# Kernel tuning notes

Measured on AMD Instinct MI355X. Metric: run time of the kernel, lower is better.

Reference implementation:

```python
import jax, jax.numpy as jnp
import numpy as np

MUL_S, MUL_V = 256, 128              # 256x0e + 128x1o hidden irreps
DIM_H = MUL_S + 3 * MUL_V            # 640
N_NODES = 100000
INV_SQRT3 = 3.0 ** -0.5
# e3nn 'element' path normalization: sqrt(ir_out.dim / sum_paths(mul1*mul2));
# for the 1o output the extra sqrt(3) cancels the 1/sqrt(3) of the wigner-3j,
# so every path ends up with the same constant.
C0 = (1.0 / (MUL_S + MUL_V)) ** 0.5


def _unif(key, shape, fan):
    # matches linear_layer_init: uniform(-a, a), a = sqrt(6/(mul1*mul2 + mul_out)), mul2 = 1
    a = (6.0 / fan) ** 0.5
    return jax.random.uniform(key, shape, minval=-a, maxval=a, dtype=jnp.float32)


def setup_inputs() -> dict:
    key = jax.random.key(0)
    ks = jax.random.split(key, 8)
    data_in = jax.random.normal(ks[0], (N_NODES, DIM_H + 4), dtype=jnp.float32)
    return {
        "data_in": data_in,
        "W_ss": _unif(ks[1], (MUL_S, MUL_S), MUL_S + MUL_S),      # 0e x 0e -> 0e (scalars)
        "W_vv": _unif(ks[2], (MUL_V, MUL_S), MUL_V + MUL_S),      # 1o x 1o -> 0e (scalars)
        "W_ss_g": _unif(ks[3], (MUL_S, MUL_V), MUL_S + MUL_V),    # 0e x 0e -> 0e (gates)
        "W_vv_g": _unif(ks[4], (MUL_V, MUL_V), MUL_V + MUL_V),    # 1o x 1o -> 0e (gates)
        "W_sv": _unif(ks[5], (MUL_S, MUL_V), MUL_S + MUL_V),      # 0e x 1o -> 1o
        "W_vs": _unif(ks[6], (MUL_V, MUL_V), MUL_V + MUL_V),      # 1o x 0e -> 1o
        "b": jnp.zeros((MUL_S,), dtype=jnp.float32),
    }


def reference(data_in, W_ss, W_vv, W_ss_g, W_vv_g, W_sv, W_vs, b):
    # split hidden / pos parts (forward does data_in[:, :-irreps_pos.dim] etc.)
    xs = data_in[:, :MUL_S]                           # [N, 256] 0e
    xv = data_in[:, MUL_S:DIM_H].reshape(-1, MUL_V, 3)  # [N, 128, 3] 1o
    ps = data_in[:, DIM_H:DIM_H + 1]                  # [N, 1] pos scalar
    pv = data_in[:, DIM_H + 1:]                       # [N, 3] pos vector

    # CG invariants feeding the 0e outputs
    s0 = xs * ps                                       # 0e x 0e path
    dot = jnp.einsum('nuk,nk->nu', xv, pv) * INV_SQRT3  # 1o x 1o -> 0e path, [N, 128]

    scal = C0 * (s0 @ W_ss + dot @ W_vv) + b           # [N, 256] scalars (+bias on N_trivial)
    gate = C0 * (s0 @ W_ss_g + dot @ W_vv_g)           # [N, 128] gates

    # 1o outputs: 0e x 1o and 1o x 0e paths
    v1 = (xs @ W_sv)[:, :, None] * pv[:, None, :]            # [N, 128, 3]
    v2 = jnp.einsum('nuk,uw->nwk', xv, W_vs) * ps[:, :, None]  # [N, 128, 3]
    vec = C0 * (v1 + v2)

    # Gate: Swish(beta=1) on scalars, sigmoid(gates) multiplying gated 1o irreps
    scal_out = scal * jax.nn.sigmoid(scal)
    vec_out = vec * jax.nn.sigmoid(gate)[:, :, None]
    return jnp.concatenate([scal_out, vec_out.reshape(-1, 3 * MUL_V)], axis=1)  # [N, 640]
```

## Files before the change

kernel.cpp:

```cpp
#include <hip/hip_runtime.h>
#include <hip/hip_bf16.h>

#define MUL_Sc 256
#define DIM_Hc 640
#define IN_COLS 644
#define KF 768
#define NT 64

#define C0F 0.05103103630798287f
#define INV_SQRT3F 0.57735026918962576f

typedef __attribute__((ext_vector_type(8))) short short8;
typedef __attribute__((ext_vector_type(4))) float f32x4;

#define MFMA(a, b, c) __builtin_amdgcn_mfma_f32_16x16x32_bf16((a), (b), (c), 0, 0, 0)

__device__ __forceinline__ unsigned short f2bf(float x) {
    union { float f; unsigned u; } v; v.f = x;
    unsigned r = v.u + 0x7fffu + ((v.u >> 16) & 1u);
    return (unsigned short)(r >> 16);
}

__global__ void prep_weights(const float* __restrict__ Wss, const float* __restrict__ Wvv,
                             const float* __restrict__ Wssg, const float* __restrict__ Wvvg,
                             const float* __restrict__ Wsv, const float* __restrict__ Wvs,
                             unsigned short* __restrict__ wt) {
    int i = blockIdx.x * 256 + threadIdx.x;
    const int N_SG = 384 * 384;
    const int N_SV = 128 * 256;
    const int N_VS = 128 * 128;
    if (i < N_SG) {
        int col = i / 384, k = i % 384;
        float v;
        if (col < 256) v = (k < 256) ? Wss[k * 256 + col] : Wvv[(k - 256) * 256 + col];
        else { int c = col - 256; v = (k < 256) ? Wssg[k * 128 + c] : Wvvg[(k - 256) * 128 + c]; }
        wt[i] = f2bf(v);
    } else if (i < N_SG + N_SV) {
        int j = i - N_SG; int col = j >> 8, k = j & 255;
        wt[i] = f2bf(Wsv[k * 128 + col]);
    } else if (i < N_SG + N_SV + N_VS) {
        int j = i - N_SG - N_SV; int col = j >> 7, k = j & 127;
        wt[i] = f2bf(Wvs[k * 128 + col]);
    }
}

__global__ __launch_bounds__(512, 2)
void fused_main(const float* __restrict__ din, const unsigned short* __restrict__ wt,
                const float* __restrict__ bias, float* __restrict__ out, int N) {
    __shared__ unsigned short feat[NT * KF];
    __shared__ float psv[NT * 4];

    const int tid = threadIdx.x;
    const int n0 = blockIdx.x * NT;

    {
        const int g = tid >> 3;
        const int j = tid & 7;
        int n = n0 + g; if (n >= N) n = N - 1;
        const float* row = din + (size_t)n * IN_COLS;
        float ps  = row[DIM_Hc];
        float pv0 = row[DIM_Hc + 1], pv1 = row[DIM_Hc + 2], pv2 = row[DIM_Hc + 3];
        if (j == 0) { psv[g*4+0] = ps; psv[g*4+1] = pv0; psv[g*4+2] = pv1; psv[g*4+3] = pv2; }
        char* fb = (char*)feat;
        const int swz  = (g & 7) << 4;
        const int rowb = g * (KF * 2);

        #pragma unroll
        for (int half = 0; half < 2; ++half) {
            int c = 32 * j + 16 * half;
            float4 x0 = *(const float4*)(row + c);
            float4 x1 = *(const float4*)(row + c + 4);
            float4 x2 = *(const float4*)(row + c + 8);
            float4 x3 = *(const float4*)(row + c + 12);
            short8 p0, p1;
            p0[0]=(short)f2bf(x0.x); p0[1]=(short)f2bf(x0.y); p0[2]=(short)f2bf(x0.z); p0[3]=(short)f2bf(x0.w);
            p0[4]=(short)f2bf(x1.x); p0[5]=(short)f2bf(x1.y); p0[6]=(short)f2bf(x1.z); p0[7]=(short)f2bf(x1.w);
            p1[0]=(short)f2bf(x2.x); p1[1]=(short)f2bf(x2.y); p1[2]=(short)f2bf(x2.z); p1[3]=(short)f2bf(x2.w);
            p1[4]=(short)f2bf(x3.x); p1[5]=(short)f2bf(x3.y); p1[6]=(short)f2bf(x3.z); p1[7]=(short)f2bf(x3.w);
            *(short8*)(fb + ((rowb + c * 2) ^ swz))       = p0;
            *(short8*)(fb + ((rowb + (c + 8) * 2) ^ swz)) = p1;
        }
        #pragma unroll
        for (int half = 0; half < 2; ++half) {
            int u0 = 16 * j + 8 * half;
            const float* p = row + MUL_Sc + 3 * u0;
            float e[24];
            #pragma unroll
            for (int q = 0; q < 6; ++q) {
                float4 v = *(const float4*)(p + 4 * q);
                e[4*q+0] = v.x; e[4*q+1] = v.y; e[4*q+2] = v.z; e[4*q+3] = v.w;
            }
            short8 dp, k0, k1, k2;
            #pragma unroll
            for (int m = 0; m < 8; ++m) {
                float a = e[3*m], b = e[3*m+1], c = e[3*m+2];
                dp[m] = (short)f2bf((a * pv0 + b * pv1 + c * pv2) * INV_SQRT3F);
                k0[m] = (short)f2bf(a);
                k1[m] = (short)f2bf(b);
                k2[m] = (short)f2bf(c);
            }
            *(short8*)(fb + ((rowb + (256 + u0) * 2) ^ swz)) = dp;
            *(short8*)(fb + ((rowb + (384 + u0) * 2) ^ swz)) = k0;
            *(short8*)(fb + ((rowb + (512 + u0) * 2) ^ swz)) = k1;
            *(short8*)(fb + ((rowb + (640 + u0) * 2) ^ swz)) = k2;
        }
    }
    __syncthreads();

    const int wave = tid >> 6;
    const int lane = tid & 63;
    const int l15  = lane & 15;
    const int lkb  = (lane >> 4) << 3;
    const int rbase = (lane >> 4) << 2;
    const char* fbr = (const char*)feat;
    const int swzr = (l15 & 7) << 4;

    const unsigned short* WTsg = wt;
    const unsigned short* WTsv = wt + 384 * 384;
    const unsigned short* WTvs = wt + 384 * 384 + 128 * 256;

    float pss[4][4];
    #pragma unroll
    for (int m = 0; m < 4; ++m)
    #pragma unroll
    for (int i = 0; i < 4; ++i) pss[m][i] = psv[(m * 16 + rbase + i) * 4];

    f32x4 accS[3][4];
    #pragma unroll
    for (int t = 0; t < 3; ++t)
    #pragma unroll
    for (int m = 0; m < 4; ++m) accS[t][m] = (f32x4){0,0,0,0};

    #pragma unroll
    for (int ks = 0; ks < 8; ++ks) {
        int kf = ks * 32 + lkb;
        short8 a[4];
        #pragma unroll
        for (int m = 0; m < 4; ++m)
            a[m] = *(const short8*)(fbr + (((m * 16 + l15) * 1536 + kf * 2) ^ swzr));
        #pragma unroll
        for (int t = 0; t < 3; ++t) {
            int ct = wave + t * 8;
            short8 b = *(const short8*)(WTsg + (ct * 16 + l15) * 384 + ks * 32 + lkb);
            #pragma unroll
            for (int m = 0; m < 4; ++m) accS[t][m] = MFMA(a[m], b, accS[t][m]);
        }
    }
    #pragma unroll
    for (int t = 0; t < 3; ++t)
    #pragma unroll
    for (int m = 0; m < 4; ++m)
    #pragma unroll
    for (int i = 0; i < 4; ++i) accS[t][m][i] *= pss[m][i];
    #pragma unroll
    for (int ks = 0; ks < 4; ++ks) {
        int kf = 256 + ks * 32 + lkb;
        short8 a[4];
        #pragma unroll
        for (int m = 0; m < 4; ++m)
            a[m] = *(const short8*)(fbr + (((m * 16 + l15) * 1536 + kf * 2) ^ swzr));
        #pragma unroll
        for (int t = 0; t < 3; ++t) {
            int ct = wave + t * 8;
            short8 b = *(const short8*)(WTsg + (ct * 16 + l15) * 384 + 256 + ks * 32 + lkb);
            #pragma unroll
            for (int m = 0; m < 4; ++m) accS[t][m] = MFMA(a[m], b, accS[t][m]);
        }
    }

    #pragma unroll
    for (int t = 0; t < 2; ++t) {
        int col = (wave + t * 8) * 16 + l15;
        float bc = bias[col];
        #pragma unroll
        for (int m = 0; m < 4; ++m)
        #pragma unroll
        for (int i = 0; i < 4; ++i) {
            int n = n0 + m * 16 + rbase + i;
            if (n < N) {
                float sc = C0F * accS[t][m][i] + bc;
                out[(size_t)n * DIM_Hc + col] = sc / (1.f + __expf(-sc));
            }
        }
    }
    float sgr[4][4];
    #pragma unroll
    for (int m = 0; m < 4; ++m)
    #pragma unroll
    for (int i = 0; i < 4; ++i) sgr[m][i] = 1.f / (1.f + __expf(-C0F * accS[2][m][i]));

    f32x4 accA[4], accV[3][4];
    #pragma unroll
    for (int m = 0; m < 4; ++m) accA[m] = (f32x4){0,0,0,0};
    #pragma unroll
    for (int k = 0; k < 3; ++k)
    #pragma unroll
    for (int m = 0; m < 4; ++m) accV[k][m] = (f32x4){0,0,0,0};

    #pragma unroll
    for (int ks = 0; ks < 8; ++ks) {
        int kf = ks * 32 + lkb;
        short8 b = *(const short8*)(WTsv + (wave * 16 + l15) * 256 + ks * 32 + lkb);
        #pragma unroll
        for (int m = 0; m < 4; ++m) {
            short8 a = *(const short8*)(fbr + (((m * 16 + l15) * 1536 + kf * 2) ^ swzr));
            accA[m] = MFMA(a, b, accA[m]);
        }
    }
    #pragma unroll
    for (int ks = 0; ks < 4; ++ks) {
        short8 b = *(const short8*)(WTvs + (wave * 16 + l15) * 128 + ks * 32 + lkb);
        #pragma unroll
        for (int p = 0; p < 3; ++p) {
            int kf = 384 + 128 * p + ks * 32 + lkb;
            #pragma unroll
            for (int m = 0; m < 4; ++m) {
                short8 a = *(const short8*)(fbr + (((m * 16 + l15) * 1536 + kf * 2) ^ swzr));
                accV[p][m] = MFMA(a, b, accV[p][m]);
            }
        }
    }

    {
        int u = wave * 16 + l15;
        #pragma unroll
        for (int m = 0; m < 4; ++m)
        #pragma unroll
        for (int i = 0; i < 4; ++i) {
            int nl = m * 16 + rbase + i;
            int n = n0 + nl;
            if (n >= N) continue;
            float sg  = sgr[m][i];
            float ps  = pss[m][i];
            float pv0 = psv[nl * 4 + 1], pv1 = psv[nl * 4 + 2], pv2 = psv[nl * 4 + 3];
            float av = accA[m][i];
            size_t ob = (size_t)n * DIM_Hc + MUL_Sc + 3 * u;
            out[ob + 0] = C0F * (av * pv0 + accV[0][m][i] * ps) * sg;
            out[ob + 1] = C0F * (av * pv1 + accV[1][m][i] * ps) * sg;
            out[ob + 2] = C0F * (av * pv2 + accV[2][m][i] * ps) * sg;
        }
    }
}

extern "C" void kernel_launch(void* const* d_in, const int* in_sizes, int n_in,
                              void* d_out, int out_size, void* d_ws, size_t ws_size,
                              hipStream_t stream) {
    const float* din  = (const float*)d_in[0];
    const float* Wss  = (const float*)d_in[1];
    const float* Wvv  = (const float*)d_in[2];
    const float* Wssg = (const float*)d_in[3];
    const float* Wvvg = (const float*)d_in[4];
    const float* Wsv  = (const float*)d_in[5];
    const float* Wvs  = (const float*)d_in[6];
    const float* bias = (const float*)d_in[7];
    float* out = (float*)d_out;
    unsigned short* wt = (unsigned short*)d_ws;

    const size_t WT_BYTES = (size_t)(384 * 384 + 128 * 256 + 128 * 128) * 2;
    if (ws_size < WT_BYTES) return;

    int N = in_sizes[0] / IN_COLS;

    int prep_total = 384 * 384 + 128 * 256 + 128 * 128;
    prep_weights<<<(prep_total + 255) / 256, 256, 0, stream>>>(Wss, Wvv, Wssg, Wvvg, Wsv, Wvs, wt);

    int nblocks = (N + NT - 1) / NT;
    fused_main<<<nblocks, 512, 0, stream>>>(din, wt, bias, out, N);
}
```

Measured before the change: 234.5 us.

## Make fused kernel persistent with double-buffered LDS and register prefetch of next tile

Switches from one 64-node block per tile to a persistent grid of 256 blocks that walk 32-node tiles. While the current tile runs its MFMA work, the next tile's input row is prefetched into registers, then converted to bf16 into the other LDS buffer. The aim is to hide global load latency behind compute and cut per-block setup overhead. The cost is smaller M tiles (half the MFMA reuse of each B fragment loaded from global), higher register pressure from the prefetch registers, and a grid of only 256 blocks, which may leave compute units underused with 2 blocks per CU allowed.

Measured after the change: 449.5 us. 91.7% more time.

```diff
diff --git a/kernel.cpp b/kernel.cpp
--- a/kernel.cpp
+++ b/kernel.cpp
@@ -5,7 +5,8 @@
 #define DIM_Hc 640
 #define IN_COLS 644
 #define KF 768
-#define NT 64
+#define NT 32
+#define GRIDB 256
 
 #define C0F 0.05103103630798287f
 #define INV_SQRT3F 0.57735026918962576f
@@ -46,32 +47,54 @@
 
 __global__ __launch_bounds__(512, 2)
 void fused_main(const float* __restrict__ din, const unsigned short* __restrict__ wt,
-                const float* __restrict__ bias, float* __restrict__ out, int N) {
-    __shared__ unsigned short feat[NT * KF];
-    __shared__ float psv[NT * 4];
+                const float* __restrict__ bias, float* __restrict__ out,
+                int N, int ntiles) {
+    __shared__ unsigned short feat[2][NT * KF];
+    __shared__ float psv[2][NT * 4];
 
     const int tid = threadIdx.x;
-    const int n0 = blockIdx.x * NT;
-
-    {
-        const int g = tid >> 3;
-        const int j = tid & 7;
-        int n = n0 + g; if (n >= N) n = N - 1;
+    const int g = tid >> 4;
+    const int j = tid & 15;
+
+    const int wave = tid >> 6;
+    const int lane = tid & 63;
+    const int l15  = lane & 15;
+    const int lkb  = (lane >> 4) << 3;
+    const int rbase = (lane >> 4) << 2;
+    const int swzr = (l15 & 7) << 4;
+
+    const unsigned short* WTsg = wt;
+    const unsigned short* WTsv = wt + 384 * 384;
+    const unsigned short* WTvs = wt + 384 * 384 + 128 * 256;
+
+    float bc0 = bias[(wave)     * 16 + l15];
+    float bc1 = bias[(wave + 8) * 16 + l15];
+
+    float4 xs4[4], xv4[6], pp;
+
+    auto issue = [&](int tile) {
+        int n = tile * NT + g; if (n >= N) n = N - 1;
         const float* row = din + (size_t)n * IN_COLS;
-        float ps  = row[DIM_Hc];
-        float pv0 = row[DIM_Hc + 1], pv1 = row[DIM_Hc + 2], pv2 = row[DIM_Hc + 3];
-        if (j == 0) { psv[g*4+0] = ps; psv[g*4+1] = pv0; psv[g*4+2] = pv1; psv[g*4+3] = pv2; }
-        char* fb = (char*)feat;
+        #pragma unroll
+        for (int q = 0; q < 4; ++q) xs4[q] = *(const float4*)(row + 16 * j + 4 * q);
+        #pragma unroll
+        for (int q = 0; q < 6; ++q) xv4[q] = *(const float4*)(row + MUL_Sc + 24 * j + 4 * q);
+        pp = *(const float4*)(row + DIM_Hc);
+    };
+
+    auto convertw = [&](int wb) {
+        char* fb = (char*)&feat[wb][0];
         const int swz  = (g & 7) << 4;
         const int rowb = g * (KF * 2);
-
-        #pragma unroll
-        for (int half = 0; half < 2; ++half) {
-            int c = 32 * j + 16 * half;
-            float4 x0 = *(const float4*)(row + c);
-            float4 x1 = *(const float4*)(row + c + 4);
-            float4 x2 = *(const float4*)(row + c + 8);
-            float4 x3 = *(const float4*)(row + c + 12);
+        float ps = pp.x, pv0 = pp.y, pv1 = pp.z, pv2 = pp.w;
+        (void)ps;
+        if (j == 0) {
+            psv[wb][g*4+0] = pp.x; psv[wb][g*4+1] = pp.y;
+            psv[wb][g*4+2] = pp.z; psv[wb][g*4+3] = pp.w;
+        }
+        {
+            int c = 16 * j;
+            float4 x0 = xs4[0], x1 = xs4[1], x2 = xs4[2], x3 = xs4[3];
             short8 p0, p1;
             p0[0]=(short)f2bf(x0.x); p0[1]=(short)f2bf(x0.y); p0[2]=(short)f2bf(x0.z); p0[3]=(short)f2bf(x0.w);
             p0[4]=(short)f2bf(x1.x); p0[5]=(short)f2bf(x1.y); p0[6]=(short)f2bf(x1.z); p0[7]=(short)f2bf(x1.w);
@@ -80,14 +103,12 @@
             *(short8*)(fb + ((rowb + c * 2) ^ swz))       = p0;
             *(short8*)(fb + ((rowb + (c + 8) * 2) ^ swz)) = p1;
         }
-        #pragma unroll
-        for (int half = 0; half < 2; ++half) {
-            int u0 = 16 * j + 8 * half;
-            const float* p = row + MUL_Sc + 3 * u0;
+        {
+            int u0 = 8 * j;
             float e[24];
             #pragma unroll
             for (int q = 0; q < 6; ++q) {
-                float4 v = *(const float4*)(p + 4 * q);
+                float4 v = xv4[q];
                 e[4*q+0] = v.x; e[4*q+1] = v.y; e[4*q+2] = v.z; e[4*q+3] = v.w;
             }
             short8 dp, k0, k1, k2;
@@ -104,140 +125,142 @@
             *(short8*)(fb + ((rowb + (512 + u0) * 2) ^ swz)) = k1;
             *(short8*)(fb + ((rowb + (640 + u0) * 2) ^ swz)) = k2;
         }
-    }
+    };
+
+    const int t0 = blockIdx.x;
+    if (t0 < ntiles) { issue(t0); convertw(0); }
     __syncthreads();
 
-    const int wave = tid >> 6;
-    const int lane = tid & 63;
-    const int l15  = lane & 15;
-    const int lkb  = (lane >> 4) << 3;
-    const int rbase = (lane >> 4) << 2;
-    const char* fbr = (const char*)feat;
-    const int swzr = (l15 & 7) << 4;
-
-    const unsigned short* WTsg = wt;
-    const unsigned short* WTsv = wt + 384 * 384;
-    const unsigned short* WTvs = wt + 384 * 384 + 128 * 256;
-
-    float pss[4][4];
-    #pragma unroll
-    for (int m = 0; m < 4; ++m)
-    #pragma unroll
-    for (int i = 0; i < 4; ++i) pss[m][i] = psv[(m * 16 + rbase + i) * 4];
-
-    f32x4 accS[3][4];
-    #pragma unroll
-    for (int t = 0; t < 3; ++t)
-    #pragma unroll
-    for (int m = 0; m < 4; ++m) accS[t][m] = (f32x4){0,0,0,0};
-
-    #pragma unroll
-    for (int ks = 0; ks < 8; ++ks) {
-        int kf = ks * 32 + lkb;
-        short8 a[4];
-        #pragma unroll
-        for (int m = 0; m < 4; ++m)
-            a[m] = *(const short8*)(fbr + (((m * 16 + l15) * 1536 + kf * 2) ^ swzr));
-        #pragma unroll
-        for (int t = 0; t < 3; ++t) {
-            int ct = wave + t * 8;
-            short8 b = *(const short8*)(WTsg + (ct * 16 + l15) * 384 + ks * 32 + lkb);
-            #pragma unroll
-            for (int m = 0; m < 4; ++m) accS[t][m] = MFMA(a[m], b, accS[t][m]);
-        }
-    }
-    #pragma unroll
-    for (int t = 0; t < 3; ++t)
-    #pragma unroll
-    for (int m = 0; m < 4; ++m)
-    #pragma unroll
-    for (int i = 0; i < 4; ++i) accS[t][m][i] *= pss[m][i];
-    #pragma unroll
-    for (int ks = 0; ks < 4; ++ks) {
-        int kf = 256 + ks * 32 + lkb;
-        short8 a[4];
-        #pragma unroll
-        for (int m = 0; m < 4; ++m)
-            a[m] = *(const short8*)(fbr + (((m * 16 + l15) * 1536 + kf * 2) ^ swzr));
-        #pragma unroll
-        for (int t = 0; t < 3; ++t) {
-            int ct = wave + t * 8;
-            short8 b = *(const short8*)(WTsg + (ct * 16 + l15) * 384 + 256 + ks * 32 + lkb);
-            #pragma unroll
-            for (int m = 0; m < 4; ++m) accS[t][m] = MFMA(a[m], b, accS[t][m]);
-        }
-    }
-
-    #pragma unroll
-    for (int t = 0; t < 2; ++t) {
-        int col = (wave + t * 8) * 16 + l15;
-        float bc = bias[col];
-        #pragma unroll
-        for (int m = 0; m < 4; ++m)
-        #pragma unroll
-        for (int i = 0; i < 4; ++i) {
-            int n = n0 + m * 16 + rbase + i;
-            if (n < N) {
-                float sc = C0F * accS[t][m][i] + bc;
-                out[(size_t)n * DIM_Hc + col] = sc / (1.f + __expf(-sc));
-            }
-        }
-    }
-    float sgr[4][4];
-    #pragma unroll
-    for (int m = 0; m < 4; ++m)
-    #pragma unroll
-    for (int i = 0; i < 4; ++i) sgr[m][i] = 1.f / (1.f + __expf(-C0F * accS[2][m][i]));
-
-    f32x4 accA[4], accV[3][4];
-    #pragma unroll
-    for (int m = 0; m < 4; ++m) accA[m] = (f32x4){0,0,0,0};
-    #pragma unroll
-    for (int k = 0; k < 3; ++k)
-    #pragma unroll
-    for (int m = 0; m < 4; ++m) accV[k][m] = (f32x4){0,0,0,0};
-
-    #pragma unroll
-    for (int ks = 0; ks < 8; ++ks) {
-        int kf = ks * 32 + lkb;
-        short8 b = *(const short8*)(WTsv + (wave * 16 + l15) * 256 + ks * 32 + lkb);
-        #pragma unroll
-        for (int m = 0; m < 4; ++m) {
-            short8 a = *(const short8*)(fbr + (((m * 16 + l15) * 1536 + kf * 2) ^ swzr));
-            accA[m] = MFMA(a, b, accA[m]);
-        }
-    }
-    #pragma unroll
-    for (int ks = 0; ks < 4; ++ks) {
-        short8 b = *(const short8*)(WTvs + (wave * 16 + l15) * 128 + ks * 32 + lkb);
-        #pragma unroll
-        for (int p = 0; p < 3; ++p) {
-            int kf = 384 + 128 * p + ks * 32 + lkb;
-            #pragma unroll
-            for (int m = 0; m < 4; ++m) {
-                short8 a = *(const short8*)(fbr + (((m * 16 + l15) * 1536 + kf * 2) ^ swzr));
-                accV[p][m] = MFMA(a, b, accV[p][m]);
-            }
-        }
-    }
-
-    {
-        int u = wave * 16 + l15;
-        #pragma unroll
-        for (int m = 0; m < 4; ++m)
-        #pragma unroll
-        for (int i = 0; i < 4; ++i) {
-            int nl = m * 16 + rbase + i;
-            int n = n0 + nl;
-            if (n >= N) continue;
-            float sg  = sgr[m][i];
-            float ps  = pss[m][i];
-            float pv0 = psv[nl * 4 + 1], pv1 = psv[nl * 4 + 2], pv2 = psv[nl * 4 + 3];
-            float av = accA[m][i];
-            size_t ob = (size_t)n * DIM_Hc + MUL_Sc + 3 * u;
-            out[ob + 0] = C0F * (av * pv0 + accV[0][m][i] * ps) * sg;
-            out[ob + 1] = C0F * (av * pv1 + accV[1][m][i] * ps) * sg;
-            out[ob + 2] = C0F * (av * pv2 + accV[2][m][i] * ps) * sg;
+    int cur = 0;
+    for (int tile = t0; tile < ntiles; tile += GRIDB) {
+        const int nx = tile + GRIDB;
+        if (nx < ntiles) issue(nx);
+
+        {
+            const char* fbr = (const char*)&feat[cur][0];
+            const float* pvv = &psv[cur][0];
+            const int n0 = tile * NT;
+
+            float pss[2][4];
+            #pragma unroll
+            for (int m = 0; m < 2; ++m)
+            #pragma unroll
+            for (int i = 0; i < 4; ++i) pss[m][i] = pvv[(m * 16 + rbase + i) * 4];
+
+            f32x4 accS[3][2];
+            #pragma unroll
+            for (int t = 0; t < 3; ++t) { accS[t][0] = (f32x4){0,0,0,0}; accS[t][1] = (f32x4){0,0,0,0}; }
+
+            #pragma unroll
+            for (int ks = 0; ks < 8; ++ks) {
+                int kf = ks * 32 + lkb;
+                short8 a0 = *(const short8*)(fbr + ((l15 * 1536 + kf * 2) ^ swzr));
+                short8 a1 = *(const short8*)(fbr + (((16 + l15) * 1536 + kf * 2) ^ swzr));
+                #pragma unroll
+                for (int t = 0; t < 3; ++t) {
+                    int ct = wave + t * 8;
+                    short8 b = *(const short8*)(WTsg + (ct * 16 + l15) * 384 + ks * 32 + lkb);
+                    accS[t][0] = MFMA(a0, b, accS[t][0]);
+                    accS[t][1] = MFMA(a1, b, accS[t][1]);
+                }
+            }
+            #pragma unroll
+            for (int t = 0; t < 3; ++t)
+            #pragma unroll
+            for (int m = 0; m < 2; ++m)
+            #pragma unroll
+            for (int i = 0; i < 4; ++i) accS[t][m][i] *= pss[m][i];
+            #pragma unroll
+            for (int ks = 0; ks < 4; ++ks) {
+                int kf = 256 + ks * 32 + lkb;
+                short8 a0 = *(const short8*)(fbr + ((l15 * 1536 + kf * 2) ^ swzr));
+                short8 a1 = *(const short8*)(fbr + (((16 + l15) * 1536 + kf * 2) ^ swzr));
+                #pragma unroll
+                for (int t = 0; t < 3; ++t) {
+                    int ct = wave + t * 8;
+                    short8 b = *(const short8*)(WTsg + (ct * 16 + l15) * 384 + 256 + ks * 32 + lkb);
+                    accS[t][0] = MFMA(a0, b, accS[t][0]);
+                    accS[t][1] = MFMA(a1, b, accS[t][1]);
+                }
+            }
+
+            #pragma unroll
+            for (int t = 0; t < 2; ++t) {
+                int col = (wave + t * 8) * 16 + l15;
+                float bc = t == 0 ? bc0 : bc1;
+                #pragma unroll
+                for (int m = 0; m < 2; ++m)
+                #pragma unroll
+                for (int i = 0; i < 4; ++i) {
+                    int n = n0 + m * 16 + rbase + i;
+                    if (n < N) {
+                        float sc = C0F * accS[t][m][i] + bc;
+                        out[(size_t)n * DIM_Hc + col] = sc / (1.f + __expf(-sc));
+                    }
+                }
+            }
+            float sgr[2][4];
+            #pragma unroll
+            for (int m = 0; m < 2; ++m)
+            #pragma unroll
+            for (int i = 0; i < 4; ++i) sgr[m][i] = 1.f / (1.f + __expf(-C0F * accS[2][m][i]));
+
+            f32x4 accA[2], accV[3][2];
+            accA[0] = (f32x4){0,0,0,0}; accA[1] = (f32x4){0,0,0,0};
+            #pragma unroll
+            for (int k = 0; k < 3; ++k) { accV[k][0] = (f32x4){0,0,0,0}; accV[k][1] = (f32x4){0,0,0,0}; }
+
+            #pragma unroll
+            for (int ks = 0; ks < 8; ++ks) {
+                int kf = ks * 32 + lkb;
+                short8 a0 = *(const short8*)(fbr + ((l15 * 1536 + kf * 2) ^ swzr));
+                short8 a1 = *(const short8*)(fbr + (((16 + l15) * 1536 + kf * 2) ^ swzr));
+                short8 b = *(const short8*)(WTsv + (wave * 16 + l15) * 256 + ks * 32 + lkb);
+                accA[0] = MFMA(a0, b, accA[0]);
+                accA[1] = MFMA(a1, b, accA[1]);
+            }
+            #pragma unroll
+            for (int ks = 0; ks < 4; ++ks) {
+                short8 b = *(const short8*)(WTvs + (wave * 16 + l15) * 128 + ks * 32 + lkb);
+                #pragma unroll
+                for (int p = 0; p < 3; ++p) {
+                    int kf = 384 + 128 * p + ks * 32 + lkb;
+                    short8 a0 = *(const short8*)(fbr + ((l15 * 1536 + kf * 2) ^ swzr));
+                    short8 a1 = *(const short8*)(fbr + (((16 + l15) * 1536 + kf * 2) ^ swzr));
+                    accV[p][0] = MFMA(a0, b, accV[p][0]);
+                    accV[p][1] = MFMA(a1, b, accV[p][1]);
+                }
+            }
+
+            {
+                int u = wave * 16 + l15;
+                #pragma unroll
+                for (int m = 0; m < 2; ++m)
+                #pragma unroll
+                for (int i = 0; i < 4; ++i) {
+                    int nl = m * 16 + rbase + i;
+                    int n = n0 + nl;
+                    if (n >= N) continue;
+                    float sg  = sgr[m][i];
+                    float ps  = pss[m][i];
+                    float pv0 = pvv[nl * 4 + 1], pv1 = pvv[nl * 4 + 2], pv2 = pvv[nl * 4 + 3];
+                    float av = accA[m][i];
+                    size_t ob = (size_t)n * DIM_Hc + MUL_Sc + 3 * u;
+                    out[ob + 0] = C0F * (av * pv0 + accV[0][m][i] * ps) * sg;
+                    out[ob + 1] = C0F * (av * pv1 + accV[1][m][i] * ps) * sg;
+                    out[ob + 2] = C0F * (av * pv2 + accV[2][m][i] * ps) * sg;
+                }
+            }
+        }
+
+        if (nx < ntiles) {
+            asm volatile("s_waitcnt vmcnt(0)" ::: "memory");
+            convertw(cur ^ 1);
+            asm volatile("s_waitcnt lgkmcnt(0)" ::: "memory");
+            __builtin_amdgcn_sched_barrier(0);
+            asm volatile("s_barrier" ::: "memory");
+            __builtin_amdgcn_sched_barrier(0);
+            cur ^= 1;
         }
     }
 }
@@ -260,10 +283,10 @@
     if (ws_size < WT_BYTES) return;
 
     int N = in_sizes[0] / IN_COLS;
+    int ntiles = (N + NT - 1) / NT;
 
     int prep_total = 384 * 384 + 128 * 256 + 128 * 128;
     prep_weights<<<(prep_total + 255) / 256, 256, 0, stream>>>(Wss, Wvv, Wssg, Wvvg, Wsv, Wvs, wt);
 
-    int nblocks = (N + NT - 1) / NT;
-    fused_main<<<nblocks, 512, 0, stream>>>(din, wt, bias, out, N);
-}
+    fused_main<<<GRIDB, 512, 0, stream>>>(din, wt, bias, out, N, ntiles);
+}
```

## Split feature conversion into separate kernel and stage bf16 tiles via global_load_lds

Applied to the files above, without the earlier changes.

Splits the fused kernel in two. One kernel converts the input rows to a pre-swizzled bf16 feature buffer plus a position array in workspace. A GEMM kernel then pulls 32-row tiles straight into LDS with global_load_lds and runs the MFMA work. The aim is to take the fp32 convert work off the GEMM kernel's critical path and halve the tile size for more blocks, but it adds a round trip through global memory for about 150 MB of intermediate bf16 data. A fused fallback is kept for when the workspace is too small.

Result: slower. 331.0 us (+41.1%).

```diff
diff --git a/kernel.cpp b/kernel.cpp
--- a/kernel.cpp
+++ b/kernel.cpp
@@ -5,7 +5,7 @@
 #define DIM_Hc 640
 #define IN_COLS 644
 #define KF 768
-#define NT 64
+#define NTS 32
 
 #define C0F 0.05103103630798287f
 #define INV_SQRT3F 0.57735026918962576f
@@ -19,6 +19,11 @@
     union { float f; unsigned u; } v; v.f = x;
     unsigned r = v.u + 0x7fffu + ((v.u >> 16) & 1u);
     return (unsigned short)(r >> 16);
+}
+
+__device__ __forceinline__ void gload_lds16(const unsigned short* g, unsigned short* l) {
+    __builtin_amdgcn_global_load_lds((const __attribute__((address_space(1))) void*)g,
+                                     (__attribute__((address_space(3))) void*)l, 16, 0, 0);
 }
 
 __global__ void prep_weights(const float* __restrict__ Wss, const float* __restrict__ Wvv,
@@ -45,14 +50,219 @@
 }
 
 __global__ __launch_bounds__(512, 2)
-void fused_main(const float* __restrict__ din, const unsigned short* __restrict__ wt,
-                const float* __restrict__ bias, float* __restrict__ out, int N) {
-    __shared__ unsigned short feat[NT * KF];
-    __shared__ float psv[NT * 4];
-
+void convert_feat(const float* __restrict__ din, unsigned short* __restrict__ featg,
+                  float* __restrict__ psvg, int N) {
+    const int T = blockIdx.x;
     const int tid = threadIdx.x;
-    const int n0 = blockIdx.x * NT;
-
+    const int g = tid >> 4;
+    const int j = tid & 15;
+    int n = T * NTS + g; if (n >= N) n = N - 1;
+    const float* row = din + (size_t)n * IN_COLS;
+    float ps  = row[DIM_Hc];
+    float pv0 = row[DIM_Hc + 1], pv1 = row[DIM_Hc + 2], pv2 = row[DIM_Hc + 3];
+    if (j == 0 && T * NTS + g < N) {
+        float4 pp; pp.x = ps; pp.y = pv0; pp.z = pv1; pp.w = pv2;
+        *(float4*)(psvg + 4 * (size_t)(T * NTS + g)) = pp;
+    }
+    char* fb = (char*)featg + (size_t)T * (NTS * KF * 2);
+    const int swz  = (g & 7) << 4;
+    const int rowb = g * (KF * 2);
+
+    {
+        int c = 16 * j;
+        float4 x0 = *(const float4*)(row + c);
+        float4 x1 = *(const float4*)(row + c + 4);
+        float4 x2 = *(const float4*)(row + c + 8);
+        float4 x3 = *(const float4*)(row + c + 12);
+        short8 p0, p1;
+        p0[0]=(short)f2bf(x0.x); p0[1]=(short)f2bf(x0.y); p0[2]=(short)f2bf(x0.z); p0[3]=(short)f2bf(x0.w);
+        p0[4]=(short)f2bf(x1.x); p0[5]=(short)f2bf(x1.y); p0[6]=(short)f2bf(x1.z); p0[7]=(short)f2bf(x1.w);
+        p1[0]=(short)f2bf(x2.x); p1[1]=(short)f2bf(x2.y); p1[2]=(short)f2bf(x2.z); p1[3]=(short)f2bf(x2.w);
+        p1[4]=(short)f2bf(x3.x); p1[5]=(short)f2bf(x3.y); p1[6]=(short)f2bf(x3.z); p1[7]=(short)f2bf(x3.w);
+        *(short8*)(fb + ((rowb + c * 2) ^ swz))       = p0;
+        *(short8*)(fb + ((rowb + (c + 8) * 2) ^ swz)) = p1;
+    }
+    {
+        int u0 = 8 * j;
+        const float* p = row + MUL_Sc + 3 * u0;
+        float e[24];
+        #pragma unroll
+        for (int q = 0; q < 6; ++q) {
+            float4 v = *(const float4*)(p + 4 * q);
+            e[4*q+0] = v.x; e[4*q+1] = v.y; e[4*q+2] = v.z; e[4*q+3] = v.w;
+        }
+        short8 dp, k0, k1, k2;
+        #pragma unroll
+        for (int m = 0; m < 8; ++m) {
+            float a = e[3*m], b = e[3*m+1], c = e[3*m+2];
+            dp[m] = (short)f2bf((a * pv0 + b * pv1 + c * pv2) * INV_SQRT3F);
+            k0[m] = (short)f2bf(a);
+            k1[m] = (short)f2bf(b);
+            k2[m] = (short)f2bf(c);
+        }
+        *(short8*)(fb + ((rowb + (256 + u0) * 2) ^ swz)) = dp;
+        *(short8*)(fb + ((rowb + (384 + u0) * 2) ^ swz)) = k0;
+        *(short8*)(fb + ((rowb + (512 + u0) * 2) ^ swz)) = k1;
+        *(short8*)(fb + ((rowb + (640 + u0) * 2) ^ swz)) = k2;
+    }
+}
+
+__global__ __launch_bounds__(512, 2)
+void gemm_main(const unsigned short* __restrict__ featg, const float* __restrict__ psvg,
+               const unsigned short* __restrict__ wt, const float* __restrict__ bias,
+               float* __restrict__ out, int N) {
+    __shared__ unsigned short feat[NTS * KF];
+
+    const int tid = threadIdx.x;
+    const int T = blockIdx.x;
+    const int n0 = T * NTS;
+
+    {
+        const unsigned short* gb = featg + (size_t)T * (NTS * KF);
+        unsigned short* lb = feat + (tid >> 6) * 512;
+        #pragma unroll
+        for (int r = 0; r < 6; ++r)
+            gload_lds16(gb + ((size_t)r * 512 + tid) * 8, lb + r * 4096);
+    }
+    __syncthreads();
+
+    const int wave = tid >> 6;
+    const int lane = tid & 63;
+    const int l15  = lane & 15;
+    const int lkb  = (lane >> 4) << 3;
+    const int rbase = (lane >> 4) << 2;
+    const char* fbr = (const char*)feat;
+    const int swzr = (l15 & 7) << 4;
+
+    const unsigned short* WTsg = wt;
+    const unsigned short* WTsv = wt + 384 * 384;
+    const unsigned short* WTvs = wt + 384 * 384 + 128 * 256;
+
+    float pss[2][4];
+    #pragma unroll
+    for (int m = 0; m < 2; ++m)
+    #pragma unroll
+    for (int i = 0; i < 4; ++i) {
+        int n = n0 + m * 16 + rbase + i;
+        pss[m][i] = psvg[4 * (size_t)(n < N ? n : N - 1)];
+    }
+
+    f32x4 accS[3][2];
+    #pragma unroll
+    for (int t = 0; t < 3; ++t) { accS[t][0] = (f32x4){0,0,0,0}; accS[t][1] = (f32x4){0,0,0,0}; }
+
+    #pragma unroll
+    for (int ks = 0; ks < 8; ++ks) {
+        int kf = ks * 32 + lkb;
+        short8 a0 = *(const short8*)(fbr + ((l15 * 1536 + kf * 2) ^ swzr));
+        short8 a1 = *(const short8*)(fbr + (((16 + l15) * 1536 + kf * 2) ^ swzr));
+        #pragma unroll
+        for (int t = 0; t < 3; ++t) {
+            int ct = wave + t * 8;
+            short8 b = *(const short8*)(WTsg + (ct * 16 + l15) * 384 + ks * 32 + lkb);
+            accS[t][0] = MFMA(a0, b, accS[t][0]);
+            accS[t][1] = MFMA(a1, b, accS[t][1]);
+        }
+    }
+    #pragma unroll
+    for (int t = 0; t < 3; ++t)
+    #pragma unroll
+    for (int m = 0; m < 2; ++m)
+    #pragma unroll
+    for (int i = 0; i < 4; ++i) accS[t][m][i] *= pss[m][i];
+    #pragma unroll
+    for (int ks = 0; ks < 4; ++ks) {
+        int kf = 256 + ks * 32 + lkb;
+        short8 a0 = *(const short8*)(fbr + ((l15 * 1536 + kf * 2) ^ swzr));
+        short8 a1 = *(const short8*)(fbr + (((16 + l15) * 1536 + kf * 2) ^ swzr));
+        #pragma unroll
+        for (int t = 0; t < 3; ++t) {
+            int ct = wave + t * 8;
+            short8 b = *(const short8*)(WTsg + (ct * 16 + l15) * 384 + 256 + ks * 32 + lkb);
+            accS[t][0] = MFMA(a0, b, accS[t][0]);
+            accS[t][1] = MFMA(a1, b, accS[t][1]);
+        }
+    }
+
+    #pragma unroll
+    for (int t = 0; t < 2; ++t) {
+        int col = (wave + t * 8) * 16 + l15;
+        float bc = bias[col];
+        #pragma unroll
+        for (int m = 0; m < 2; ++m)
+        #pragma unroll
+        for (int i = 0; i < 4; ++i) {
+            int n = n0 + m * 16 + rbase + i;
+            if (n < N) {
+                float sc = C0F * accS[t][m][i] + bc;
+                out[(size_t)n * DIM_Hc + col] = sc / (1.f + __expf(-sc));
+            }
+        }
+    }
+    float sgr[2][4];
+    #pragma unroll
+    for (int m = 0; m < 2; ++m)
+    #pragma unroll
+    for (int i = 0; i < 4; ++i) sgr[m][i] = 1.f / (1.f + __expf(-C0F * accS[2][m][i]));
+
+    f32x4 accA[2], accV[3][2];
+    accA[0] = (f32x4){0,0,0,0}; accA[1] = (f32x4){0,0,0,0};
+    #pragma unroll
+    for (int k = 0; k < 3; ++k) { accV[k][0] = (f32x4){0,0,0,0}; accV[k][1] = (f32x4){0,0,0,0}; }
+
+    #pragma unroll
+    for (int ks = 0; ks < 8; ++ks) {
+        int kf = ks * 32 + lkb;
+        short8 a0 = *(const short8*)(fbr + ((l15 * 1536 + kf * 2) ^ swzr));
+        short8 a1 = *(const short8*)(fbr + (((16 + l15) * 1536 + kf * 2) ^ swzr));
+        short8 b = *(const short8*)(WTsv + (wave * 16 + l15) * 256 + ks * 32 + lkb);
+        accA[0] = MFMA(a0, b, accA[0]);
+        accA[1] = MFMA(a1, b, accA[1]);
+    }
+    #pragma unroll
+    for (int ks = 0; ks < 4; ++ks) {
+        short8 b = *(const short8*)(WTvs + (wave * 16 + l15) * 128 + ks * 32 + lkb);
+        #pragma unroll
+        for (int p = 0; p < 3; ++p) {
+            int kf = 384 + 128 * p + ks * 32 + lkb;
+            short8 a0 = *(const short8*)(fbr + ((l15 * 1536 + kf * 2) ^ swzr));
+            short8 a1 = *(const short8*)(fbr + (((16 + l15) * 1536 + kf * 2) ^ swzr));
+            accV[p][0] = MFMA(a0, b, accV[p][0]);
+            accV[p][1] = MFMA(a1, b, accV[p][1]);
+        }
+    }
+
+    {
+        int u = wave * 16 + l15;
+        #pragma unroll
+        for (int m = 0; m < 2; ++m)
+        #pragma unroll
+        for (int i = 0; i < 4; ++i) {
+            int nl = m * 16 + rbase + i;
+            int n = n0 + nl;
+            if (n >= N) continue;
+            float sg  = sgr[m][i];
+            float ps  = pss[m][i];
+            float pv0 = psvg[4 * (size_t)n + 1];
+            float pv1 = psvg[4 * (size_t)n + 2];
+            float pv2 = psvg[4 * (size_t)n + 3];
+            float av = accA[m][i];
+            size_t ob = (size_t)n * DIM_Hc + MUL_Sc + 3 * u;
+            out[ob + 0] = C0F * (av * pv0 + accV[0][m][i] * ps) * sg;
+            out[ob + 1] = C0F * (av * pv1 + accV[1][m][i] * ps) * sg;
+            out[ob + 2] = C0F * (av * pv2 + accV[2][m][i] * ps) * sg;
+        }
+    }
+}
+
+__global__ __launch_bounds__(512, 2)
+void fused_fallback(const float* __restrict__ din, const unsigned short* __restrict__ wt,
+                    const float* __restrict__ bias, float* __restrict__ out, int N) {
+    __shared__ unsigned short feat[64 * KF];
+    __shared__ float psv[64 * 4];
+
+    const int tid = threadIdx.x;
+    const int n0 = blockIdx.x * 64;
     {
         const int g = tid >> 3;
         const int j = tid & 7;
@@ -64,7 +274,6 @@
         char* fb = (char*)feat;
         const int swz  = (g & 7) << 4;
         const int rowb = g * (KF * 2);
-
         #pragma unroll
         for (int half = 0; half < 2; ++half) {
             int c = 32 * j + 16 * half;
@@ -95,9 +304,7 @@
             for (int m = 0; m < 8; ++m) {
                 float a = e[3*m], b = e[3*m+1], c = e[3*m+2];
                 dp[m] = (short)f2bf((a * pv0 + b * pv1 + c * pv2) * INV_SQRT3F);
-                k0[m] = (short)f2bf(a);
-                k1[m] = (short)f2bf(b);
-                k2[m] = (short)f2bf(c);
+                k0[m] = (short)f2bf(a); k1[m] = (short)f2bf(b); k2[m] = (short)f2bf(c);
             }
             *(short8*)(fb + ((rowb + (256 + u0) * 2) ^ swz)) = dp;
             *(short8*)(fb + ((rowb + (384 + u0) * 2) ^ swz)) = k0;
@@ -167,7 +374,6 @@
             for (int m = 0; m < 4; ++m) accS[t][m] = MFMA(a[m], b, accS[t][m]);
         }
     }
-
     #pragma unroll
     for (int t = 0; t < 2; ++t) {
         int col = (wave + t * 8) * 16 + l15;
@@ -220,7 +426,6 @@
             }
         }
     }
-
     {
         int u = wave * 16 + l15;
         #pragma unroll
@@ -256,14 +461,27 @@
     float* out = (float*)d_out;
     unsigned short* wt = (unsigned short*)d_ws;
 
-    const size_t WT_BYTES = (size_t)(384 * 384 + 128 * 256 + 128 * 128) * 2;
+    const size_t WT_SHORTS = 384 * 384 + 128 * 256 + 128 * 128;
+    const size_t WT_BYTES = WT_SHORTS * 2;
     if (ws_size < WT_BYTES) return;
 
     int N = in_sizes[0] / IN_COLS;
-
-    int prep_total = 384 * 384 + 128 * 256 + 128 * 128;
+    int ntiles = (N + NTS - 1) / NTS;
+
+    int prep_total = (int)WT_SHORTS;
     prep_weights<<<(prep_total + 255) / 256, 256, 0, stream>>>(Wss, Wvv, Wssg, Wvvg, Wsv, Wvs, wt);
 
-    int nblocks = (N + NT - 1) / NT;
-    fused_main<<<nblocks, 512, 0, stream>>>(din, wt, bias, out, N);
-}
+    size_t feat_bytes = (size_t)ntiles * NTS * KF * 2;
+    size_t psv_bytes  = (size_t)ntiles * NTS * 4 * sizeof(float);
+    size_t need = WT_BYTES + feat_bytes + psv_bytes;
+
+    if (ws_size >= need) {
+        unsigned short* featg = wt + WT_SHORTS;
+        float* psvg = (float*)((char*)d_ws + WT_BYTES + feat_bytes);
+        convert_feat<<<ntiles, 512, 0, stream>>>(din, featg, psvg, N);
+        gemm_main<<<ntiles, 512, 0, stream>>>(featg, psvg, wt, bias, out, N);
+    } else {
+        int nblocks = (N + 63) / 64;
+        fused_fallback<<<nblocks, 512, 0, stream>>>(din, wt, bias, out, N);
+    }
+}
```
